# Kernel optimization log

Hardware: AMD Instinct MI355X
Metric: run time of the kernel (lower is better)

The kernel has to match this reference:

```python
import jax, jax.numpy as jnp
import numpy as np

N_NODES = 200000
N_EDGES = 6400000


def setup_inputs() -> dict:
    key = jax.random.key(0)
    ks = jax.random.split(key, 10)
    x = jax.random.normal(ks[0], (N_NODES, 3), dtype=jnp.float32)
    edge_index = jax.random.randint(ks[1], (2, N_EDGES), 0, N_NODES, dtype=jnp.int64)
    # PyG SAGEConv params: lin_l applied to mean-aggregated neighbors (has bias),
    # lin_r applied to root features (no bias).
    def lin(k, fin, fout):
        return jax.random.normal(k, (fin, fout), dtype=jnp.float32) / jnp.sqrt(fin)
    W1l = lin(ks[2], 3, 32)
    W1r = lin(ks[3], 3, 32)
    b1 = jnp.zeros((32,), dtype=jnp.float32)
    W2l = lin(ks[4], 32, 16)
    W2r = lin(ks[5], 32, 16)
    b2 = jnp.zeros((16,), dtype=jnp.float32)
    Wlin = lin(ks[6], 16, 2)
    blin = jnp.zeros((2,), dtype=jnp.float32)
    return {"x": x, "edge_index": edge_index, "W1l": W1l, "W1r": W1r, "b1": b1,
            "W2l": W2l, "W2r": W2r, "b2": b2, "Wlin": Wlin, "blin": blin}


def _sage_conv(x, src, dst, Wl, Wr, b):
    # mean-aggregate neighbor features: messages flow src -> dst
    msg_sum = jax.ops.segment_sum(x[src], dst, num_segments=N_NODES)  # [N, F]
    cnt = jax.ops.segment_sum(jnp.ones_like(dst, dtype=x.dtype), dst, num_segments=N_NODES)
    mean = msg_sum / jnp.maximum(cnt, 1.0)[:, None]
    return mean @ Wl + x @ Wr + b


def reference(x, edge_index, W1l, W1r, b1, W2l, W2r, b2, Wlin, blin):
    src, dst = edge_index[0], edge_index[1]
    h = jax.nn.relu(_sage_conv(x, src, dst, W1l, W1r, b1))   # [N, 32]
    h = _sage_conv(h, src, dst, W2l, W2r, b2)                # [N, 16]
    return h @ Wlin + blin                                   # [N, 2]
```

## Files before the change

kernel.cpp:

```cpp
#include <hip/hip_runtime.h>


#define NB 512
#define BTILE 392
#define CAP 24
#define SRCB 18
#define SRCMASK ((1u << SRCB) - 1u)
#define PH 8192

typedef __fp16 half2v __attribute__((ext_vector_type(2)));

static __device__ __forceinline__ unsigned pkrtz(float a, float b) {
    half2v h = __builtin_amdgcn_cvt_pkrtz(a, b);
    return __builtin_bit_cast(unsigned, h);
}
static __device__ __forceinline__ float2 unpk(unsigned u) {
    half2v h = __builtin_bit_cast(half2v, u);
    return make_float2((float)h.x, (float)h.y);
}
static __device__ __forceinline__ void lds_pk_add(unsigned* p, unsigned pk) {
    unsigned off = (unsigned)(size_t)p;
    asm volatile("ds_pk_add_f16 %0, %1" :: "v"(off), "v"(pk) : "memory");
}

__global__ void precomp_kernel(const float* __restrict__ W2l, const float* __restrict__ W2r,
                               const float* __restrict__ b2, const float* __restrict__ Wlin,
                               const float* __restrict__ blin, float* __restrict__ ABc) {
    int t = threadIdx.x;
    if (t < 64) {
        int r = t >> 1, c = t & 1;
        float sA = 0.f, sB = 0.f;
        for (int k = 0; k < 16; ++k) {
            float w = Wlin[k * 2 + c];
            sA += W2l[r * 16 + k] * w;
            sB += W2r[r * 16 + k] * w;
        }
        ABc[t] = sA;
        ABc[64 + t] = sB;
    } else if (t < 66) {
        int c = t - 64;
        float s = blin[c];
        for (int k = 0; k < 16; ++k) s += b2[k] * Wlin[k * 2 + c];
        ABc[128 + c] = s;
    }
}

__global__ void xpad_kernel(const float* __restrict__ x, uint2* __restrict__ xh, int N) {
    int n = blockIdx.x * 256 + threadIdx.x;
    if (n < N) {
        float x0 = x[3 * (size_t)n], x1 = x[3 * (size_t)n + 1], x2 = x[3 * (size_t)n + 2];
        xh[n] = make_uint2(pkrtz(x0, x1), pkrtz(x2, 1.0f));
    }
}

__global__ __launch_bounds__(512) void hist_kernel(const int* __restrict__ dst,
        unsigned* __restrict__ hist, int E, int ECB) {
    __shared__ unsigned lh[NB];
    const int tid = threadIdx.x;
    for (int i = tid; i < NB; i += 512) lh[i] = 0;
    __syncthreads();
    int e0 = blockIdx.x * ECB; if (e0 > E) e0 = E;
    int e1 = e0 + ECB;         if (e1 > E) e1 = E;
    int nv = (e1 - e0) >> 2;
    const int4* d4 = (const int4*)(dst + e0);
    for (int i = tid; i < nv; i += 512) {
        int4 d = d4[i];
        atomicAdd(&lh[(unsigned)d.x / (unsigned)BTILE], 1u);
        atomicAdd(&lh[(unsigned)d.y / (unsigned)BTILE], 1u);
        atomicAdd(&lh[(unsigned)d.z / (unsigned)BTILE], 1u);
        atomicAdd(&lh[(unsigned)d.w / (unsigned)BTILE], 1u);
    }
    for (int e = e0 + (nv << 2) + tid; e < e1; e += 512)
        atomicAdd(&lh[(unsigned)dst[e] / (unsigned)BTILE], 1u);
    __syncthreads();
    for (int i = tid; i < NB; i += 512) if (lh[i]) atomicAdd(&hist[i], lh[i]);
}

__global__ void scan_kernel(const unsigned* __restrict__ hist,
                            unsigned* __restrict__ offsets, unsigned* __restrict__ cursor) {
    __shared__ unsigned s[NB];
    int t = threadIdx.x;
    unsigned v = hist[t];
    s[t] = v;
    __syncthreads();
    for (int d = 1; d < NB; d <<= 1) {
        unsigned u = (t >= d) ? s[t - d] : 0u;
        __syncthreads();
        s[t] += u;
        __syncthreads();
    }
    unsigned excl = s[t] - v;
    offsets[t] = excl;
    cursor[t] = excl;
}

__global__ __launch_bounds__(512) void bin_kernel(const int* __restrict__ src,
        const int* __restrict__ dst, unsigned* __restrict__ records,
        unsigned* __restrict__ cursor, int E, int ECB) {
    __shared__ unsigned stage[NB * CAP];
    __shared__ unsigned lcnt[NB];
    __shared__ unsigned gbase[NB];
    const int tid = threadIdx.x;
    int e0 = blockIdx.x * ECB; if (e0 > E) e0 = E;
    int e1 = e0 + ECB;         if (e1 > E) e1 = E;

    for (int ph = e0; ph < e1; ph += PH) {
        int pe = ph + PH; if (pe > e1) pe = e1;
        for (int i = tid; i < NB; i += 512) lcnt[i] = 0;
        __syncthreads();
        int p = ph + tid * 16;
#define BINPROC(dd, ss) { unsigned d_ = (unsigned)(dd);                                    \
        unsigned b_ = d_ / (unsigned)BTILE;                                                \
        unsigned r_ = d_ - b_ * (unsigned)BTILE;                                           \
        unsigned rec_ = (r_ << SRCB) | (unsigned)(ss);                                     \
        unsigned pos_ = atomicAdd(&lcnt[b_], 1u);                                          \
        if (pos_ < (unsigned)CAP) stage[b_ * CAP + pos_] = rec_;                           \
        else { unsigned gp_ = atomicAdd(&cursor[b_], 1u); records[gp_] = rec_; } }
        if (p + 16 <= pe) {
            int4 d0 = *(const int4*)(dst + p);      int4 d1 = *(const int4*)(dst + p + 4);
            int4 d2 = *(const int4*)(dst + p + 8);  int4 d3 = *(const int4*)(dst + p + 12);
            int4 s0 = *(const int4*)(src + p);      int4 s1 = *(const int4*)(src + p + 4);
            int4 s2 = *(const int4*)(src + p + 8);  int4 s3 = *(const int4*)(src + p + 12);
            BINPROC(d0.x, s0.x); BINPROC(d0.y, s0.y); BINPROC(d0.z, s0.z); BINPROC(d0.w, s0.w);
            BINPROC(d1.x, s1.x); BINPROC(d1.y, s1.y); BINPROC(d1.z, s1.z); BINPROC(d1.w, s1.w);
            BINPROC(d2.x, s2.x); BINPROC(d2.y, s2.y); BINPROC(d2.z, s2.z); BINPROC(d2.w, s2.w);
            BINPROC(d3.x, s3.x); BINPROC(d3.y, s3.y); BINPROC(d3.z, s3.z); BINPROC(d3.w, s3.w);
        } else {
            for (int e = p; e < pe; ++e) BINPROC(dst[e], src[e]);
        }
#undef BINPROC
        __syncthreads();
        if (tid < NB) {
            unsigned c = lcnt[tid]; if (c > (unsigned)CAP) c = CAP;
            gbase[tid] = c ? atomicAdd(&cursor[tid], c) : 0u;
        }
        __syncthreads();
        for (int j = tid; j < NB * CAP; j += 512) {
            unsigned bb = (unsigned)j / (unsigned)CAP;
            unsigned kk = (unsigned)j - bb * (unsigned)CAP;
            unsigned c = lcnt[bb]; if (c > (unsigned)CAP) c = CAP;
            if (kk < c) records[gbase[bb] + kk] = stage[j];
        }
        __syncthreads();
    }
}

template<int USEXH>
__global__ __launch_bounds__(1024, 8) void b1_kernel(const unsigned* __restrict__ records,
        const unsigned* __restrict__ offsets, const unsigned* __restrict__ hist,
        const float* __restrict__ x, const uint2* __restrict__ xh,
        const float* __restrict__ W1l, const float* __restrict__ W1r,
        const float* __restrict__ b1, const float* __restrict__ ABc,
        unsigned* __restrict__ g1h, float* __restrict__ hB,
        float* __restrict__ invArr, int N) {
    __shared__ unsigned accXY[BTILE], accZW[BTILE];
    __shared__ float sW1l[96], sW1r[96], sb1[32], sA[64], sB[64];
    const int tid = threadIdx.x;
    const int b = blockIdx.x;
    for (int i = tid; i < BTILE; i += 1024) { accXY[i] = 0u; accZW[i] = 0u; }
    if (tid < 96) { sW1l[tid] = W1l[tid]; sW1r[tid] = W1r[tid]; }
    else if (tid < 128) sb1[tid - 96] = b1[tid - 96];
    else if (tid < 192) sA[tid - 128] = ABc[tid - 128];
    else if (tid < 256) sB[tid - 192] = ABc[tid - 192 + 64];
    __syncthreads();
    const int start = (int)offsets[b];
    const int end = start + (int)hist[b];
    int i = start + tid;
    for (; i + 3072 < end; i += 4096) {
        unsigned r[4];
        uint2 p[4];
#pragma unroll
        for (int k = 0; k < 4; ++k) r[k] = records[i + k * 1024];
#pragma unroll
        for (int k = 0; k < 4; ++k) {
            unsigned s = r[k] & SRCMASK;
            if (USEXH) p[k] = xh[s];
            else { float3 v = *(const float3*)(x + 3 * (size_t)s);
                   p[k] = make_uint2(pkrtz(v.x, v.y), pkrtz(v.z, 1.0f)); }
        }
#pragma unroll
        for (int k = 0; k < 4; ++k) {
            unsigned rr = r[k] >> SRCB;
            lds_pk_add(&accXY[rr], p[k].x);
            lds_pk_add(&accZW[rr], p[k].y);
        }
    }
    for (; i < end; i += 1024) {
        unsigned rc = records[i];
        unsigned s = rc & SRCMASK;
        uint2 pv;
        if (USEXH) pv = xh[s];
        else { float3 v = *(const float3*)(x + 3 * (size_t)s);
               pv = make_uint2(pkrtz(v.x, v.y), pkrtz(v.z, 1.0f)); }
        unsigned rr = rc >> SRCB;
        lds_pk_add(&accXY[rr], pv.x);
        lds_pk_add(&accZW[rr], pv.y);
    }
    asm volatile("s_waitcnt lgkmcnt(0)" ::: "memory");
    __syncthreads();
    if (tid < BTILE) {
        int n = b * BTILE + tid;
        if (n < N) {
            float2 xy = unpk(accXY[tid]);
            float2 zw = unpk(accZW[tid]);
            float inv = 1.0f / fmaxf(zw.y, 1.0f);
            float m0 = xy.x * inv, m1 = xy.y * inv, m2 = zw.x * inv;
            float x0 = x[3 * (size_t)n], x1 = x[3 * (size_t)n + 1], x2 = x[3 * (size_t)n + 2];
            float gA0 = 0.f, gA1 = 0.f, gB0 = 0.f, gB1 = 0.f;
#pragma unroll
            for (int k = 0; k < 32; ++k) {
                float h = m0 * sW1l[k] + m1 * sW1l[32 + k] + m2 * sW1l[64 + k]
                        + x0 * sW1r[k] + x1 * sW1r[32 + k] + x2 * sW1r[64 + k] + sb1[k];
                h = fmaxf(h, 0.0f);
                gA0 += h * sA[2 * k];     gA1 += h * sA[2 * k + 1];
                gB0 += h * sB[2 * k];     gB1 += h * sB[2 * k + 1];
            }
            g1h[n] = pkrtz(gA0, gA1);
            *(float2*)(hB + 2 * (size_t)n) = make_float2(gB0, gB1);
            invArr[n] = inv;
        }
    }
}

__global__ __launch_bounds__(1024, 8) void b2_kernel(const unsigned* __restrict__ records,
        const unsigned* __restrict__ offsets, const unsigned* __restrict__ hist,
        const unsigned* __restrict__ g1h, const float* __restrict__ hB,
        const float* __restrict__ invArr, const float* __restrict__ ABc,
        float* __restrict__ out, int N) {
    __shared__ unsigned accXY[BTILE];
    const int tid = threadIdx.x;
    const int b = blockIdx.x;
    for (int i = tid; i < BTILE; i += 1024) accXY[i] = 0u;
    __syncthreads();
    const int start = (int)offsets[b];
    const int end = start + (int)hist[b];
    int i = start + tid;
    for (; i + 3072 < end; i += 4096) {
        unsigned r[4];
        unsigned g[4];
#pragma unroll
        for (int k = 0; k < 4; ++k) r[k] = records[i + k * 1024];
#pragma unroll
        for (int k = 0; k < 4; ++k) g[k] = g1h[r[k] & SRCMASK];
#pragma unroll
        for (int k = 0; k < 4; ++k) lds_pk_add(&accXY[r[k] >> SRCB], g[k]);
    }
    for (; i < end; i += 1024) {
        unsigned rc = records[i];
        unsigned g = g1h[rc & SRCMASK];
        lds_pk_add(&accXY[rc >> SRCB], g);
    }
    asm volatile("s_waitcnt lgkmcnt(0)" ::: "memory");
    __syncthreads();
    if (tid < BTILE) {
        int n = b * BTILE + tid;
        if (n < N) {
            float2 s = unpk(accXY[tid]);
            float inv = invArr[n];
            float2 hb = *(const float2*)(hB + 2 * (size_t)n);
            float c0 = ABc[128], c1 = ABc[129];
            *(float2*)(out + 2 * (size_t)n) = make_float2(s.x * inv + hb.x + c0,
                                                          s.y * inv + hb.y + c1);
        }
    }
}

#define NCHUNK1 8
#define NCHUNK2 16
#define TILE1 3136
#define NTILE1 64
#define TILE2 6272
#define NTILE2 32

__global__ __launch_bounds__(512) void tile1_kernel(const int* __restrict__ src,
        const int* __restrict__ dst, const float* __restrict__ x,
        float* __restrict__ partials1, int N, int E, int EC) {
    __shared__ float acc[TILE1 * 4];
    const int tid = threadIdx.x;
    const int chunk = blockIdx.x & (NCHUNK1 - 1);
    const int base = (blockIdx.x >> 3) * TILE1;
    for (int i = tid; i < TILE1 * 4; i += 512) acc[i] = 0.f;
    __syncthreads();
    int e0 = chunk * EC; if (e0 > E) e0 = E;
    int e1 = e0 + EC;    if (e1 > E) e1 = E;
#define PROC1(dd, ss) { unsigned r = (unsigned)(dd) - (unsigned)base;            \
    if (r < (unsigned)TILE1) { const float* xp = x + 3 * (size_t)(unsigned)(ss); \
        atomicAdd(&acc[r * 4 + 0], xp[0]); atomicAdd(&acc[r * 4 + 1], xp[1]);    \
        atomicAdd(&acc[r * 4 + 2], xp[2]); atomicAdd(&acc[r * 4 + 3], 1.0f); } }
    for (int p = e0 + tid * 8; p + 7 < e1; p += 512 * 8) {
        int4 d0 = *(const int4*)(dst + p);
        int4 d1 = *(const int4*)(dst + p + 4);
        int4 s0 = *(const int4*)(src + p);
        int4 s1 = *(const int4*)(src + p + 4);
        PROC1(d0.x, s0.x); PROC1(d0.y, s0.y); PROC1(d0.z, s0.z); PROC1(d0.w, s0.w);
        PROC1(d1.x, s1.x); PROC1(d1.y, s1.y); PROC1(d1.z, s1.z); PROC1(d1.w, s1.w);
    }
    int t0 = e1 - ((e1 - e0) & 7);
    for (int e = t0 + tid; e < e1; e += 512) PROC1(dst[e], src[e]);
#undef PROC1
    __syncthreads();
    float* p = partials1 + ((size_t)chunk * N + base) * 4;
    int lim = N - base; if (lim > TILE1) lim = TILE1;
    for (int i = tid; i < lim; i += 512)
        *(float4*)(p + (size_t)i * 4) = *(const float4*)(acc + i * 4);
}

__global__ void node1t_kernel(const float* __restrict__ partials1, const float* __restrict__ x,
                              const float* __restrict__ W1l, const float* __restrict__ W1r,
                              const float* __restrict__ b1, const float* __restrict__ ABc,
                              float* __restrict__ g1, float* __restrict__ hB,
                              float* __restrict__ invArr, int N) {
    __shared__ float sW1l[96], sW1r[96], sb1[32], sA[64], sB[64];
    int tid = threadIdx.x;
    for (int i = tid; i < 96; i += 256) { sW1l[i] = W1l[i]; sW1r[i] = W1r[i]; }
    for (int i = tid; i < 32; i += 256) sb1[i] = b1[i];
    for (int i = tid; i < 64; i += 256) { sA[i] = ABc[i]; sB[i] = ABc[64 + i]; }
    __syncthreads();
    int n = blockIdx.x * 256 + tid;
    if (n >= N) return;
    float sx = 0.f, sy = 0.f, sz = 0.f, cw = 0.f;
#pragma unroll
    for (int c = 0; c < NCHUNK1; ++c) {
        float4 v = *(const float4*)(partials1 + ((size_t)c * N + n) * 4);
        sx += v.x; sy += v.y; sz += v.z; cw += v.w;
    }
    float inv = 1.0f / fmaxf(cw, 1.0f);
    float m0 = sx * inv, m1 = sy * inv, m2 = sz * inv;
    float x0 = x[3 * (size_t)n], x1 = x[3 * (size_t)n + 1], x2 = x[3 * (size_t)n + 2];
    float gA0 = 0.f, gA1 = 0.f, gB0 = 0.f, gB1 = 0.f;
#pragma unroll
    for (int k = 0; k < 32; ++k) {
        float h = m0 * sW1l[k] + m1 * sW1l[32 + k] + m2 * sW1l[64 + k]
                + x0 * sW1r[k] + x1 * sW1r[32 + k] + x2 * sW1r[64 + k] + sb1[k];
        h = fmaxf(h, 0.0f);
        gA0 += h * sA[2 * k];     gA1 += h * sA[2 * k + 1];
        gB0 += h * sB[2 * k];     gB1 += h * sB[2 * k + 1];
    }
    *(float2*)(g1 + 2 * (size_t)n) = make_float2(gA0, gA1);
    *(float2*)(hB + 2 * (size_t)n) = make_float2(gB0, gB1);
    invArr[n] = inv;
}

__global__ __launch_bounds__(512) void tile2_kernel(const int* __restrict__ src,
        const int* __restrict__ dst, const float* __restrict__ g1,
        float* __restrict__ partials2, int N, int E, int EC) {
    __shared__ float acc[TILE2 * 2];
    const int tid = threadIdx.x;
    const int chunk = blockIdx.x & (NCHUNK2 - 1);
    const int base = (blockIdx.x >> 4) * TILE2;
    for (int i = tid; i < TILE2 * 2; i += 512) acc[i] = 0.f;
    __syncthreads();
    int e0 = chunk * EC; if (e0 > E) e0 = E;
    int e1 = e0 + EC;    if (e1 > E) e1 = E;
#define PROC2(dd, ss) { unsigned r = (unsigned)(dd) - (unsigned)base;            \
    if (r < (unsigned)TILE2) {                                                   \
        float2 g = *(const float2*)(g1 + 2 * (size_t)(unsigned)(ss));            \
        atomicAdd(&acc[r * 2 + 0], g.x); atomicAdd(&acc[r * 2 + 1], g.y); } }
    for (int p = e0 + tid * 8; p + 7 < e1; p += 512 * 8) {
        int4 d0 = *(const int4*)(dst + p);
        int4 d1 = *(const int4*)(dst + p + 4);
        int4 s0 = *(const int4*)(src + p);
        int4 s1 = *(const int4*)(src + p + 4);
        PROC2(d0.x, s0.x); PROC2(d0.y, s0.y); PROC2(d0.z, s0.z); PROC2(d0.w, s0.w);
        PROC2(d1.x, s1.x); PROC2(d1.y, s1.y); PROC2(d1.z, s1.z); PROC2(d1.w, s1.w);
    }
    int t0 = e1 - ((e1 - e0) & 7);
    for (int e = t0 + tid; e < e1; e += 512) PROC2(dst[e], src[e]);
#undef PROC2
    __syncthreads();
    float* p = partials2 + ((size_t)chunk * N + base) * 2;
    int lim = N - base; if (lim > TILE2) lim = TILE2;
    for (int i = tid; i < lim; i += 512)
        *(float2*)(p + (size_t)i * 2) = *(const float2*)(acc + i * 2);
}

__global__ void node2t_kernel(const float* __restrict__ partials2, const float* __restrict__ invArr,
                              const float* __restrict__ hB, const float* __restrict__ ABc,
                              float* __restrict__ out, int N) {
    int n = blockIdx.x * 256 + threadIdx.x;
    if (n >= N) return;
    float c0 = ABc[128], c1 = ABc[129];
    float s0 = 0.f, s1 = 0.f;
#pragma unroll
    for (int c = 0; c < NCHUNK2; ++c) {
        float2 v = *(const float2*)(partials2 + ((size_t)c * N + n) * 2);
        s0 += v.x; s1 += v.y;
    }
    float inv = invArr[n];
    float2 b = *(const float2*)(hB + 2 * (size_t)n);
    *(float2*)(out + 2 * (size_t)n) = make_float2(s0 * inv + b.x + c0,
                                                  s1 * inv + b.y + c1);
}

__global__ void edge1_kernel(const int* __restrict__ src, const int* __restrict__ dst,
                             const float* __restrict__ x, float* __restrict__ agg1, int E) {
    int stride = gridDim.x * blockDim.x;
    for (int e = blockIdx.x * blockDim.x + threadIdx.x; e < E; e += stride) {
        int s = src[e], d = dst[e];
        float* p = agg1 + 4 * (size_t)d;
        atomicAdd(p + 0, x[3 * s]);
        atomicAdd(p + 1, x[3 * s + 1]);
        atomicAdd(p + 2, x[3 * s + 2]);
        atomicAdd(p + 3, 1.0f);
    }
}

__global__ void node1f_kernel(const float* __restrict__ agg1, const float* __restrict__ x,
                              const float* __restrict__ W1l, const float* __restrict__ W1r,
                              const float* __restrict__ b1, const float* __restrict__ ABc,
                              float* __restrict__ g1, float* __restrict__ hB, int N) {
    __shared__ float sW1l[96], sW1r[96], sb1[32], sA[64], sB[64];
    int tid = threadIdx.x, bs = blockDim.x;
    for (int i = tid; i < 96; i += bs) { sW1l[i] = W1l[i]; sW1r[i] = W1r[i]; }
    for (int i = tid; i < 32; i += bs) sb1[i] = b1[i];
    for (int i = tid; i < 64; i += bs) { sA[i] = ABc[i]; sB[i] = ABc[64 + i]; }
    __syncthreads();
    int stride = gridDim.x * bs;
    for (int n = blockIdx.x * bs + tid; n < N; n += stride) {
        float4 a = *(const float4*)(agg1 + 4 * (size_t)n);
        float inv = 1.0f / fmaxf(a.w, 1.0f);
        float m0 = a.x * inv, m1 = a.y * inv, m2 = a.z * inv;
        float x0 = x[3 * n], x1 = x[3 * n + 1], x2 = x[3 * n + 2];
        float gA0 = 0.f, gA1 = 0.f, gB0 = 0.f, gB1 = 0.f;
#pragma unroll
        for (int k = 0; k < 32; ++k) {
            float h = m0 * sW1l[k] + m1 * sW1l[32 + k] + m2 * sW1l[64 + k]
                    + x0 * sW1r[k] + x1 * sW1r[32 + k] + x2 * sW1r[64 + k] + sb1[k];
            h = fmaxf(h, 0.0f);
            gA0 += h * sA[2 * k];     gA1 += h * sA[2 * k + 1];
            gB0 += h * sB[2 * k];     gB1 += h * sB[2 * k + 1];
        }
        *(float2*)(g1 + 2 * (size_t)n) = make_float2(gA0, gA1);
        *(float2*)(hB + 2 * (size_t)n) = make_float2(gB0, gB1);
    }
}

__global__ void edge2_kernel(const int* __restrict__ src, const int* __restrict__ dst,
                             const float* __restrict__ g1, float* __restrict__ agg2, int E) {
    int stride = gridDim.x * blockDim.x;
    for (int e = blockIdx.x * blockDim.x + threadIdx.x; e < E; e += stride) {
        int s = src[e], d = dst[e];
        float2 g = *(const float2*)(g1 + 2 * (size_t)s);
        atomicAdd(agg2 + 2 * (size_t)d + 0, g.x);
        atomicAdd(agg2 + 2 * (size_t)d + 1, g.y);
    }
}

__global__ void node2f_kernel(const float* __restrict__ agg1, const float* __restrict__ agg2,
                              const float* __restrict__ hB, const float* __restrict__ ABc,
                              float* __restrict__ out, int N) {
    float c0 = ABc[128], c1 = ABc[129];
    int stride = gridDim.x * blockDim.x;
    for (int n = blockIdx.x * blockDim.x + threadIdx.x; n < N; n += stride) {
        float inv = 1.0f / fmaxf(agg1[4 * (size_t)n + 3], 1.0f);
        float2 a = *(const float2*)(agg2 + 2 * (size_t)n);
        float2 b = *(const float2*)(hB + 2 * (size_t)n);
        *(float2*)(out + 2 * (size_t)n) = make_float2(a.x * inv + b.x + c0,
                                                      a.y * inv + b.y + c1);
    }
}

extern "C" void kernel_launch(void* const* d_in, const int* in_sizes, int n_in,
                              void* d_out, int out_size, void* d_ws, size_t ws_size,
                              hipStream_t stream) {
    const float* x    = (const float*)d_in[0];
    const int*   ei   = (const int*)d_in[1];
    const float* W1l  = (const float*)d_in[2];
    const float* W1r  = (const float*)d_in[3];
    const float* b1   = (const float*)d_in[4];
    const float* W2l  = (const float*)d_in[5];
    const float* W2r  = (const float*)d_in[6];
    const float* b2   = (const float*)d_in[7];
    const float* Wlin = (const float*)d_in[8];
    const float* blin = (const float*)d_in[9];
    float* out = (float*)d_out;

    const int N = in_sizes[0] / 3;
    const int E = in_sizes[1] / 2;
    const int* src = ei;
    const int* dst = ei + E;

    bool common_ok = (N <= NB * BTILE) && (N <= (1 << SRCB)) && ((E & 3) == 0);

    size_t hdr   = (size_t)E + 3 * (size_t)NB;
    size_t wordsA = hdr + 2 * (size_t)N
                  + (size_t)N
                  + 3 * (size_t)N + 130;
    size_t wordsB = hdr + (size_t)N + 3 * (size_t)N + 130;

    if (common_ok && ws_size >= wordsA * 4) {
        unsigned* records = (unsigned*)d_ws;
        unsigned* hist    = records + (size_t)E;
        unsigned* offsets = hist + NB;
        unsigned* cursor  = offsets + NB;
        uint2*    xh      = (uint2*)(cursor + NB);
        unsigned* g1h     = (unsigned*)(xh + (size_t)N);
        float*    hB      = (float*)(g1h + (size_t)N);
        float*    inv     = hB + 2 * (size_t)N;
        float*    ABc     = inv + (size_t)N;

        int ECB = (((E + NB - 1) / NB) + 15) & ~15;

        hipMemsetAsync(hist, 0, NB * sizeof(unsigned), stream);
        precomp_kernel<<<1, 128, 0, stream>>>(W2l, W2r, b2, Wlin, blin, ABc);
        xpad_kernel<<<(N + 255) / 256, 256, 0, stream>>>(x, xh, N);
        hist_kernel<<<NB, 512, 0, stream>>>(dst, hist, E, ECB);
        scan_kernel<<<1, NB, 0, stream>>>(hist, offsets, cursor);
        bin_kernel <<<NB, 512, 0, stream>>>(src, dst, records, cursor, E, ECB);
        b1_kernel<1><<<NB, 1024, 0, stream>>>(records, offsets, hist, x, xh,
                                              W1l, W1r, b1, ABc, g1h, hB, inv, N);
        b2_kernel<<<NB, 1024, 0, stream>>>(records, offsets, hist, g1h, hB, inv, ABc, out, N);
        return;
    }
    if (common_ok && ws_size >= wordsB * 4) {
        unsigned* records = (unsigned*)d_ws;
        unsigned* hist    = records + (size_t)E;
        unsigned* offsets = hist + NB;
        unsigned* cursor  = offsets + NB;
        unsigned* g1h     = cursor + NB;
        float*    hB      = (float*)(g1h + (size_t)N);
        float*    inv     = hB + 2 * (size_t)N;
        float*    ABc     = inv + (size_t)N;

        int ECB = (((E + NB - 1) / NB) + 15) & ~15;

        hipMemsetAsync(hist, 0, NB * sizeof(unsigned), stream);
        precomp_kernel<<<1, 128, 0, stream>>>(W2l, W2r, b2, Wlin, blin, ABc);
        hist_kernel<<<NB, 512, 0, stream>>>(dst, hist, E, ECB);
        scan_kernel<<<1, NB, 0, stream>>>(hist, offsets, cursor);
        bin_kernel <<<NB, 512, 0, stream>>>(src, dst, records, cursor, E, ECB);
        b1_kernel<0><<<NB, 1024, 0, stream>>>(records, offsets, hist, x, nullptr,
                                              W1l, W1r, b1, ABc, g1h, hB, inv, N);
        b2_kernel<<<NB, 1024, 0, stream>>>(records, offsets, hist, g1h, hB, inv, ABc, out, N);
        return;
    }

    int EC1 = (((E + NCHUNK1 - 1) / NCHUNK1) + 15) & ~15;
    int EC2 = (((E + NCHUNK2 - 1) / NCHUNK2) + 15) & ~15;
    size_t tiled_words = 32 * (size_t)N + 5 * (size_t)N + 130;
    if (ws_size >= tiled_words * 4 && N <= NTILE1 * TILE1 && N <= NTILE2 * TILE2) {
        float* ws  = (float*)d_ws;
        float* P   = ws;
        float* g1  = ws + 32 * (size_t)N;
        float* hB  = g1 + 2 * (size_t)N;
        float* inv = hB + 2 * (size_t)N;
        float* ABc = inv + (size_t)N;
        int nb = (N + 255) / 256;
        precomp_kernel<<<1, 128, 0, stream>>>(W2l, W2r, b2, Wlin, blin, ABc);
        tile1_kernel <<<NTILE1 * NCHUNK1, 512, 0, stream>>>(src, dst, x, P, N, E, EC1);
        node1t_kernel<<<nb, 256, 0, stream>>>(P, x, W1l, W1r, b1, ABc, g1, hB, inv, N);
        tile2_kernel <<<NTILE2 * NCHUNK2, 512, 0, stream>>>(src, dst, g1, P, N, E, EC2);
        node2t_kernel<<<nb, 256, 0, stream>>>(P, inv, hB, ABc, out, N);
        return;
    }

    {
        float* ws   = (float*)d_ws;
        float* agg1 = ws;
        float* agg2 = ws + (size_t)4 * N;
        float* g1   = ws + (size_t)6 * N;
        float* hB   = ws + (size_t)8 * N;
        float* ABc  = ws + (size_t)10 * N;
        int eblocks = (E + 255) / 256;
        if (eblocks > 6144) eblocks = 6144;
        int nblocks = (N + 255) / 256;
        hipMemsetAsync(agg1, 0, (size_t)6 * N * sizeof(float), stream);
        precomp_kernel<<<1, 128, 0, stream>>>(W2l, W2r, b2, Wlin, blin, ABc);
        edge1_kernel<<<eblocks, 256, 0, stream>>>(src, dst, x, agg1, E);
        node1f_kernel<<<nblocks, 256, 0, stream>>>(agg1, x, W1l, W1r, b1, ABc, g1, hB, N);
        edge2_kernel<<<eblocks, 256, 0, stream>>>(src, dst, g1, agg2, E);
        node2f_kernel<<<nblocks, 256, 0, stream>>>(agg1, agg2, hB, ABc, out, N);
    }
}
```

Baseline: 185.5 us.

## Bin edges into fixed-capacity regions, dropping histogram, scan and xpad passes

The binning plan now gives each destination bin a fixed region of REG slots, with the cursor initialised in precomp. This removes the memset, histogram and scan kernels, and the per-bin end is read from the final cursor. The padded half-precision x copy is dropped and features are gathered straight from x. Both aggregation kernels unroll to 8 records per thread, and the memory clobber is removed from the LDS packed-add asm. The cost is a larger workspace, a reg_ok guard against bin overflow, and removal of the tiled fallback path.

```diff
diff --git a/kernel.cpp b/kernel.cpp
--- a/kernel.cpp
+++ b/kernel.cpp
@@ -3,6 +3,7 @@
 
 #define NB 512
 #define BTILE 392
+#define REG 13280
 #define CAP 24
 #define SRCB 18
 #define SRCMASK ((1u << SRCB) - 1u)
@@ -20,12 +21,14 @@
 }
 static __device__ __forceinline__ void lds_pk_add(unsigned* p, unsigned pk) {
     unsigned off = (unsigned)(size_t)p;
-    asm volatile("ds_pk_add_f16 %0, %1" :: "v"(off), "v"(pk) : "memory");
-}
-
-__global__ void precomp_kernel(const float* __restrict__ W2l, const float* __restrict__ W2r,
-                               const float* __restrict__ b2, const float* __restrict__ Wlin,
-                               const float* __restrict__ blin, float* __restrict__ ABc) {
+    asm volatile("ds_pk_add_f16 %0, %1" :: "v"(off), "v"(pk));
+}
+
+__global__ __launch_bounds__(512) void precomp_kernel(
+        const float* __restrict__ W2l, const float* __restrict__ W2r,
+        const float* __restrict__ b2, const float* __restrict__ Wlin,
+        const float* __restrict__ blin, float* __restrict__ ABc,
+        unsigned* __restrict__ cursor, int initCursor) {
     int t = threadIdx.x;
     if (t < 64) {
         int r = t >> 1, c = t & 1;
@@ -43,14 +46,7 @@
         for (int k = 0; k < 16; ++k) s += b2[k] * Wlin[k * 2 + c];
         ABc[128 + c] = s;
     }
-}
-
-__global__ void xpad_kernel(const float* __restrict__ x, uint2* __restrict__ xh, int N) {
-    int n = blockIdx.x * 256 + threadIdx.x;
-    if (n < N) {
-        float x0 = x[3 * (size_t)n], x1 = x[3 * (size_t)n + 1], x2 = x[3 * (size_t)n + 2];
-        xh[n] = make_uint2(pkrtz(x0, x1), pkrtz(x2, 1.0f));
-    }
+    if (initCursor && t < NB) cursor[t] = (unsigned)t * (unsigned)REG;
 }
 
 __global__ __launch_bounds__(512) void hist_kernel(const int* __restrict__ dst,
@@ -145,10 +141,10 @@
     }
 }
 
-template<int USEXH>
+template<int FIXEDREG>
 __global__ __launch_bounds__(1024, 8) void b1_kernel(const unsigned* __restrict__ records,
-        const unsigned* __restrict__ offsets, const unsigned* __restrict__ hist,
-        const float* __restrict__ x, const uint2* __restrict__ xh,
+        const unsigned* __restrict__ offsets, const unsigned* __restrict__ histOrEnds,
+        const float* __restrict__ x,
         const float* __restrict__ W1l, const float* __restrict__ W1r,
         const float* __restrict__ b1, const float* __restrict__ ABc,
         unsigned* __restrict__ g1h, float* __restrict__ hB,
@@ -163,23 +159,22 @@
     else if (tid < 192) sA[tid - 128] = ABc[tid - 128];
     else if (tid < 256) sB[tid - 192] = ABc[tid - 192 + 64];
     __syncthreads();
-    const int start = (int)offsets[b];
-    const int end = start + (int)hist[b];
+    int start, end;
+    if (FIXEDREG) { start = b * REG; end = (int)histOrEnds[b]; }
+    else          { start = (int)offsets[b]; end = start + (int)histOrEnds[b]; }
     int i = start + tid;
-    for (; i + 3072 < end; i += 4096) {
-        unsigned r[4];
-        uint2 p[4];
-#pragma unroll
-        for (int k = 0; k < 4; ++k) r[k] = records[i + k * 1024];
-#pragma unroll
-        for (int k = 0; k < 4; ++k) {
-            unsigned s = r[k] & SRCMASK;
-            if (USEXH) p[k] = xh[s];
-            else { float3 v = *(const float3*)(x + 3 * (size_t)s);
-                   p[k] = make_uint2(pkrtz(v.x, v.y), pkrtz(v.z, 1.0f)); }
-        }
-#pragma unroll
-        for (int k = 0; k < 4; ++k) {
+#define GATH(rc_, pv_) { unsigned s_ = (rc_) & SRCMASK;                                    \
+    float3 v_ = *(const float3*)(x + 3 * (size_t)s_);                                      \
+    pv_ = make_uint2(pkrtz(v_.x, v_.y), pkrtz(v_.z, 1.0f)); }
+    for (; i + 7168 < end; i += 8192) {
+        unsigned r[8];
+        uint2 p[8];
+#pragma unroll
+        for (int k = 0; k < 8; ++k) r[k] = records[i + k * 1024];
+#pragma unroll
+        for (int k = 0; k < 8; ++k) GATH(r[k], p[k]);
+#pragma unroll
+        for (int k = 0; k < 8; ++k) {
             unsigned rr = r[k] >> SRCB;
             lds_pk_add(&accXY[rr], p[k].x);
             lds_pk_add(&accZW[rr], p[k].y);
@@ -187,15 +182,13 @@
     }
     for (; i < end; i += 1024) {
         unsigned rc = records[i];
-        unsigned s = rc & SRCMASK;
         uint2 pv;
-        if (USEXH) pv = xh[s];
-        else { float3 v = *(const float3*)(x + 3 * (size_t)s);
-               pv = make_uint2(pkrtz(v.x, v.y), pkrtz(v.z, 1.0f)); }
+        GATH(rc, pv);
         unsigned rr = rc >> SRCB;
         lds_pk_add(&accXY[rr], pv.x);
         lds_pk_add(&accZW[rr], pv.y);
     }
+#undef GATH
     asm volatile("s_waitcnt lgkmcnt(0)" ::: "memory");
     __syncthreads();
     if (tid < BTILE) {
@@ -222,8 +215,9 @@
     }
 }
 
+template<int FIXEDREG>
 __global__ __launch_bounds__(1024, 8) void b2_kernel(const unsigned* __restrict__ records,
-        const unsigned* __restrict__ offsets, const unsigned* __restrict__ hist,
+        const unsigned* __restrict__ offsets, const unsigned* __restrict__ histOrEnds,
         const unsigned* __restrict__ g1h, const float* __restrict__ hB,
         const float* __restrict__ invArr, const float* __restrict__ ABc,
         float* __restrict__ out, int N) {
@@ -232,18 +226,19 @@
     const int b = blockIdx.x;
     for (int i = tid; i < BTILE; i += 1024) accXY[i] = 0u;
     __syncthreads();
-    const int start = (int)offsets[b];
-    const int end = start + (int)hist[b];
+    int start, end;
+    if (FIXEDREG) { start = b * REG; end = (int)histOrEnds[b]; }
+    else          { start = (int)offsets[b]; end = start + (int)histOrEnds[b]; }
     int i = start + tid;
-    for (; i + 3072 < end; i += 4096) {
-        unsigned r[4];
-        unsigned g[4];
-#pragma unroll
-        for (int k = 0; k < 4; ++k) r[k] = records[i + k * 1024];
-#pragma unroll
-        for (int k = 0; k < 4; ++k) g[k] = g1h[r[k] & SRCMASK];
-#pragma unroll
-        for (int k = 0; k < 4; ++k) lds_pk_add(&accXY[r[k] >> SRCB], g[k]);
+    for (; i + 7168 < end; i += 8192) {
+        unsigned r[8];
+        unsigned g[8];
+#pragma unroll
+        for (int k = 0; k < 8; ++k) r[k] = records[i + k * 1024];
+#pragma unroll
+        for (int k = 0; k < 8; ++k) g[k] = g1h[r[k] & SRCMASK];
+#pragma unroll
+        for (int k = 0; k < 8; ++k) lds_pk_add(&accXY[r[k] >> SRCB], g[k]);
     }
     for (; i < end; i += 1024) {
         unsigned rc = records[i];
@@ -263,133 +258,6 @@
                                                           s.y * inv + hb.y + c1);
         }
     }
-}
-
-#define NCHUNK1 8
-#define NCHUNK2 16
-#define TILE1 3136
-#define NTILE1 64
-#define TILE2 6272
-#define NTILE2 32
-
-__global__ __launch_bounds__(512) void tile1_kernel(const int* __restrict__ src,
-        const int* __restrict__ dst, const float* __restrict__ x,
-        float* __restrict__ partials1, int N, int E, int EC) {
-    __shared__ float acc[TILE1 * 4];
-    const int tid = threadIdx.x;
-    const int chunk = blockIdx.x & (NCHUNK1 - 1);
-    const int base = (blockIdx.x >> 3) * TILE1;
-    for (int i = tid; i < TILE1 * 4; i += 512) acc[i] = 0.f;
-    __syncthreads();
-    int e0 = chunk * EC; if (e0 > E) e0 = E;
-    int e1 = e0 + EC;    if (e1 > E) e1 = E;
-#define PROC1(dd, ss) { unsigned r = (unsigned)(dd) - (unsigned)base;            \
-    if (r < (unsigned)TILE1) { const float* xp = x + 3 * (size_t)(unsigned)(ss); \
-        atomicAdd(&acc[r * 4 + 0], xp[0]); atomicAdd(&acc[r * 4 + 1], xp[1]);    \
-        atomicAdd(&acc[r * 4 + 2], xp[2]); atomicAdd(&acc[r * 4 + 3], 1.0f); } }
-    for (int p = e0 + tid * 8; p + 7 < e1; p += 512 * 8) {
-        int4 d0 = *(const int4*)(dst + p);
-        int4 d1 = *(const int4*)(dst + p + 4);
-        int4 s0 = *(const int4*)(src + p);
-        int4 s1 = *(const int4*)(src + p + 4);
-        PROC1(d0.x, s0.x); PROC1(d0.y, s0.y); PROC1(d0.z, s0.z); PROC1(d0.w, s0.w);
-        PROC1(d1.x, s1.x); PROC1(d1.y, s1.y); PROC1(d1.z, s1.z); PROC1(d1.w, s1.w);
-    }
-    int t0 = e1 - ((e1 - e0) & 7);
-    for (int e = t0 + tid; e < e1; e += 512) PROC1(dst[e], src[e]);
-#undef PROC1
-    __syncthreads();
-    float* p = partials1 + ((size_t)chunk * N + base) * 4;
-    int lim = N - base; if (lim > TILE1) lim = TILE1;
-    for (int i = tid; i < lim; i += 512)
-        *(float4*)(p + (size_t)i * 4) = *(const float4*)(acc + i * 4);
-}
-
-__global__ void node1t_kernel(const float* __restrict__ partials1, const float* __restrict__ x,
-                              const float* __restrict__ W1l, const float* __restrict__ W1r,
-                              const float* __restrict__ b1, const float* __restrict__ ABc,
-                              float* __restrict__ g1, float* __restrict__ hB,
-                              float* __restrict__ invArr, int N) {
-    __shared__ float sW1l[96], sW1r[96], sb1[32], sA[64], sB[64];
-    int tid = threadIdx.x;
-    for (int i = tid; i < 96; i += 256) { sW1l[i] = W1l[i]; sW1r[i] = W1r[i]; }
-    for (int i = tid; i < 32; i += 256) sb1[i] = b1[i];
-    for (int i = tid; i < 64; i += 256) { sA[i] = ABc[i]; sB[i] = ABc[64 + i]; }
-    __syncthreads();
-    int n = blockIdx.x * 256 + tid;
-    if (n >= N) return;
-    float sx = 0.f, sy = 0.f, sz = 0.f, cw = 0.f;
-#pragma unroll
-    for (int c = 0; c < NCHUNK1; ++c) {
-        float4 v = *(const float4*)(partials1 + ((size_t)c * N + n) * 4);
-        sx += v.x; sy += v.y; sz += v.z; cw += v.w;
-    }
-    float inv = 1.0f / fmaxf(cw, 1.0f);
-    float m0 = sx * inv, m1 = sy * inv, m2 = sz * inv;
-    float x0 = x[3 * (size_t)n], x1 = x[3 * (size_t)n + 1], x2 = x[3 * (size_t)n + 2];
-    float gA0 = 0.f, gA1 = 0.f, gB0 = 0.f, gB1 = 0.f;
-#pragma unroll
-    for (int k = 0; k < 32; ++k) {
-        float h = m0 * sW1l[k] + m1 * sW1l[32 + k] + m2 * sW1l[64 + k]
-                + x0 * sW1r[k] + x1 * sW1r[32 + k] + x2 * sW1r[64 + k] + sb1[k];
-        h = fmaxf(h, 0.0f);
-        gA0 += h * sA[2 * k];     gA1 += h * sA[2 * k + 1];
-        gB0 += h * sB[2 * k];     gB1 += h * sB[2 * k + 1];
-    }
-    *(float2*)(g1 + 2 * (size_t)n) = make_float2(gA0, gA1);
-    *(float2*)(hB + 2 * (size_t)n) = make_float2(gB0, gB1);
-    invArr[n] = inv;
-}
-
-__global__ __launch_bounds__(512) void tile2_kernel(const int* __restrict__ src,
-        const int* __restrict__ dst, const float* __restrict__ g1,
-        float* __restrict__ partials2, int N, int E, int EC) {
-    __shared__ float acc[TILE2 * 2];
-    const int tid = threadIdx.x;
-    const int chunk = blockIdx.x & (NCHUNK2 - 1);
-    const int base = (blockIdx.x >> 4) * TILE2;
-    for (int i = tid; i < TILE2 * 2; i += 512) acc[i] = 0.f;
-    __syncthreads();
-    int e0 = chunk * EC; if (e0 > E) e0 = E;
-    int e1 = e0 + EC;    if (e1 > E) e1 = E;
-#define PROC2(dd, ss) { unsigned r = (unsigned)(dd) - (unsigned)base;            \
-    if (r < (unsigned)TILE2) {                                                   \
-        float2 g = *(const float2*)(g1 + 2 * (size_t)(unsigned)(ss));            \
-        atomicAdd(&acc[r * 2 + 0], g.x); atomicAdd(&acc[r * 2 + 1], g.y); } }
-    for (int p = e0 + tid * 8; p + 7 < e1; p += 512 * 8) {
-        int4 d0 = *(const int4*)(dst + p);
-        int4 d1 = *(const int4*)(dst + p + 4);
-        int4 s0 = *(const int4*)(src + p);
-        int4 s1 = *(const int4*)(src + p + 4);
-        PROC2(d0.x, s0.x); PROC2(d0.y, s0.y); PROC2(d0.z, s0.z); PROC2(d0.w, s0.w);
-        PROC2(d1.x, s1.x); PROC2(d1.y, s1.y); PROC2(d1.z, s1.z); PROC2(d1.w, s1.w);
-    }
-    int t0 = e1 - ((e1 - e0) & 7);
-    for (int e = t0 + tid; e < e1; e += 512) PROC2(dst[e], src[e]);
-#undef PROC2
-    __syncthreads();
-    float* p = partials2 + ((size_t)chunk * N + base) * 2;
-    int lim = N - base; if (lim > TILE2) lim = TILE2;
-    for (int i = tid; i < lim; i += 512)
-        *(float2*)(p + (size_t)i * 2) = *(const float2*)(acc + i * 2);
-}
-
-__global__ void node2t_kernel(const float* __restrict__ partials2, const float* __restrict__ invArr,
-                              const float* __restrict__ hB, const float* __restrict__ ABc,
-                              float* __restrict__ out, int N) {
-    int n = blockIdx.x * 256 + threadIdx.x;
-    if (n >= N) return;
-    float c0 = ABc[128], c1 = ABc[129];
-    float s0 = 0.f, s1 = 0.f;
-#pragma unroll
-    for (int c = 0; c < NCHUNK2; ++c) {
-        float2 v = *(const float2*)(partials2 + ((size_t)c * N + n) * 2);
-        s0 += v.x; s1 += v.y;
-    }
-    float inv = invArr[n];
-    float2 b = *(const float2*)(hB + 2 * (size_t)n);
-    *(float2*)(out + 2 * (size_t)n) = make_float2(s0 * inv + b.x + c0,
-                                                  s1 * inv + b.y + c1);
 }
 
 __global__ void edge1_kernel(const int* __restrict__ src, const int* __restrict__ dst,
@@ -481,37 +349,30 @@
     const int* dst = ei + E;
 
     bool common_ok = (N <= NB * BTILE) && (N <= (1 << SRCB)) && ((E & 3) == 0);
-
-    size_t hdr   = (size_t)E + 3 * (size_t)NB;
-    size_t wordsA = hdr + 2 * (size_t)N
-                  + (size_t)N
-                  + 3 * (size_t)N + 130;
-    size_t wordsB = hdr + (size_t)N + 3 * (size_t)N + 130;
-
-    if (common_ok && ws_size >= wordsA * 4) {
+    int ECB = (((E + NB - 1) / NB) + 15) & ~15;
+
+    bool reg_ok = ((E + NB - 1) / NB) + 768 <= REG;
+    size_t wordsNew = (size_t)NB * REG + NB
+                    + 4 * (size_t)N + 130;
+    if (common_ok && reg_ok && ws_size >= wordsNew * 4) {
         unsigned* records = (unsigned*)d_ws;
-        unsigned* hist    = records + (size_t)E;
-        unsigned* offsets = hist + NB;
-        unsigned* cursor  = offsets + NB;
-        uint2*    xh      = (uint2*)(cursor + NB);
-        unsigned* g1h     = (unsigned*)(xh + (size_t)N);
+        unsigned* cursor  = records + (size_t)NB * REG;
+        unsigned* g1h     = cursor + NB;
         float*    hB      = (float*)(g1h + (size_t)N);
         float*    inv     = hB + 2 * (size_t)N;
         float*    ABc     = inv + (size_t)N;
 
-        int ECB = (((E + NB - 1) / NB) + 15) & ~15;
-
-        hipMemsetAsync(hist, 0, NB * sizeof(unsigned), stream);
-        precomp_kernel<<<1, 128, 0, stream>>>(W2l, W2r, b2, Wlin, blin, ABc);
-        xpad_kernel<<<(N + 255) / 256, 256, 0, stream>>>(x, xh, N);
-        hist_kernel<<<NB, 512, 0, stream>>>(dst, hist, E, ECB);
-        scan_kernel<<<1, NB, 0, stream>>>(hist, offsets, cursor);
+        precomp_kernel<<<1, 512, 0, stream>>>(W2l, W2r, b2, Wlin, blin, ABc, cursor, 1);
         bin_kernel <<<NB, 512, 0, stream>>>(src, dst, records, cursor, E, ECB);
-        b1_kernel<1><<<NB, 1024, 0, stream>>>(records, offsets, hist, x, xh,
+        b1_kernel<1><<<NB, 1024, 0, stream>>>(records, nullptr, cursor, x,
                                               W1l, W1r, b1, ABc, g1h, hB, inv, N);
-        b2_kernel<<<NB, 1024, 0, stream>>>(records, offsets, hist, g1h, hB, inv, ABc, out, N);
+        b2_kernel<1><<<NB, 1024, 0, stream>>>(records, nullptr, cursor, g1h, hB, inv,
+                                              ABc, out, N);
         return;
     }
+
+    size_t hdr   = (size_t)E + 3 * (size_t)NB;
+    size_t wordsB = hdr + 4 * (size_t)N + 130;
     if (common_ok && ws_size >= wordsB * 4) {
         unsigned* records = (unsigned*)d_ws;
         unsigned* hist    = records + (size_t)E;
@@ -522,35 +383,15 @@
         float*    inv     = hB + 2 * (size_t)N;
         float*    ABc     = inv + (size_t)N;
 
-        int ECB = (((E + NB - 1) / NB) + 15) & ~15;
-
         hipMemsetAsync(hist, 0, NB * sizeof(unsigned), stream);
-        precomp_kernel<<<1, 128, 0, stream>>>(W2l, W2r, b2, Wlin, blin, ABc);
+        precomp_kernel<<<1, 512, 0, stream>>>(W2l, W2r, b2, Wlin, blin, ABc, cursor, 0);
         hist_kernel<<<NB, 512, 0, stream>>>(dst, hist, E, ECB);
         scan_kernel<<<1, NB, 0, stream>>>(hist, offsets, cursor);
         bin_kernel <<<NB, 512, 0, stream>>>(src, dst, records, cursor, E, ECB);
-        b1_kernel<0><<<NB, 1024, 0, stream>>>(records, offsets, hist, x, nullptr,
+        b1_kernel<0><<<NB, 1024, 0, stream>>>(records, offsets, hist, x,
                                               W1l, W1r, b1, ABc, g1h, hB, inv, N);
-        b2_kernel<<<NB, 1024, 0, stream>>>(records, offsets, hist, g1h, hB, inv, ABc, out, N);
-        return;
-    }
-
-    int EC1 = (((E + NCHUNK1 - 1) / NCHUNK1) + 15) & ~15;
-    int EC2 = (((E + NCHUNK2 - 1) / NCHUNK2) + 15) & ~15;
-    size_t tiled_words = 32 * (size_t)N + 5 * (size_t)N + 130;
-    if (ws_size >= tiled_words * 4 && N <= NTILE1 * TILE1 && N <= NTILE2 * TILE2) {
-        float* ws  = (float*)d_ws;
-        float* P   = ws;
-        float* g1  = ws + 32 * (size_t)N;
-        float* hB  = g1 + 2 * (size_t)N;
-        float* inv = hB + 2 * (size_t)N;
-        float* ABc = inv + (size_t)N;
-        int nb = (N + 255) / 256;
-        precomp_kernel<<<1, 128, 0, stream>>>(W2l, W2r, b2, Wlin, blin, ABc);
-        tile1_kernel <<<NTILE1 * NCHUNK1, 512, 0, stream>>>(src, dst, x, P, N, E, EC1);
-        node1t_kernel<<<nb, 256, 0, stream>>>(P, x, W1l, W1r, b1, ABc, g1, hB, inv, N);
-        tile2_kernel <<<NTILE2 * NCHUNK2, 512, 0, stream>>>(src, dst, g1, P, N, E, EC2);
-        node2t_kernel<<<nb, 256, 0, stream>>>(P, inv, hB, ABc, out, N);
+        b2_kernel<0><<<NB, 1024, 0, stream>>>(records, offsets, hist, g1h, hB, inv,
+                                              ABc, out, N);
         return;
     }
 
@@ -565,7 +406,8 @@
         if (eblocks > 6144) eblocks = 6144;
         int nblocks = (N + 255) / 256;
         hipMemsetAsync(agg1, 0, (size_t)6 * N * sizeof(float), stream);
-        precomp_kernel<<<1, 128, 0, stream>>>(W2l, W2r, b2, Wlin, blin, ABc);
+        precomp_kernel<<<1, 512, 0, stream>>>(W2l, W2r, b2, Wlin, blin, ABc,
+                                              (unsigned*)ws, 0);
         edge1_kernel<<<eblocks, 256, 0, stream>>>(src, dst, x, agg1, E);
         node1f_kernel<<<nblocks, 256, 0, stream>>>(agg1, x, W1l, W1r, b1, ABc, g1, hB, N);
         edge2_kernel<<<eblocks, 256, 0, stream>>>(src, dst, g1, agg2, E);
```

Result: faster. 167.1 us (-9.9%).
